# Optimization experiments

Hardware: AMD Instinct MI355X
Metric: run time of the kernel (lower is better)

Reference implementation:

```python
import jax, jax.numpy as jnp
import numpy as np

B, S, D_IN, D_OUT = 4, 2048, 4096, 4096


def setup_inputs() -> dict:
    key = jax.random.key(0)
    k1, k2, k3, k4 = jax.random.split(key, 4)
    x = jax.random.normal(k1, (B, S, D_IN), dtype=jnp.float32)
    # int8-valued weights stored as int32 (values in [-127, 127])
    weight_int8 = jax.random.randint(k2, (D_OUT, D_IN), -127, 128, dtype=jnp.int32)
    # per-output-channel scale, strictly positive (abs-max / 127 style)
    scale = jax.random.uniform(k3, (D_OUT, 1), dtype=jnp.float32, minval=1e-4, maxval=2e-2)
    bias = jax.random.normal(k4, (D_OUT,), dtype=jnp.float32)
    return {"x": x, "weight_int8": weight_int8, "scale": scale, "bias": bias}


def reference(x, weight_int8, scale, bias):
    # Dequantize: per-output-row scale applied to int8 weights -> fp32 [O, I]
    w = weight_int8.astype(jnp.float32) * scale
    # F.linear: y = x @ w^T + b
    out = jnp.einsum('bsi,oi->bso', x, w) + bias
    return out
```

## Files before the change

### kernel.cpp

```cpp
#include <hip/hip_runtime.h>
#include <cstdint>
#include <cstddef>

typedef int i32x4 __attribute__((ext_vector_type(4)));

#define BM 256
#define BN 256
#define BK 64

__device__ __forceinline__ void load16_to_lds(const void* g, void* l) {
  __builtin_amdgcn_global_load_lds(
      (const __attribute__((address_space(1))) void*)g,
      (__attribute__((address_space(3))) void*)l,
      16, 0, 0);
}

__global__ __launch_bounds__(256) void quant_xw(const float* __restrict__ x,
                                                char* __restrict__ xq,
                                                float* __restrict__ sx,
                                                const int* __restrict__ w,
                                                char* __restrict__ wq,
                                                int M, int K) {
  const int t = threadIdx.x;
  __shared__ float red[4];
  if ((int)blockIdx.x < M) {
    const int row = blockIdx.x;
    const float* xr = x + (size_t)row * K;
    float4 v[4];
    float amax = 0.f;
#pragma unroll
    for (int j = 0; j < 4; ++j) {
      v[j] = ((const float4*)xr)[t + j * 256];
      amax = fmaxf(amax, fmaxf(fmaxf(fabsf(v[j].x), fabsf(v[j].y)),
                               fmaxf(fabsf(v[j].z), fabsf(v[j].w))));
    }
#pragma unroll
    for (int off = 32; off; off >>= 1)
      amax = fmaxf(amax, __shfl_xor(amax, off));
    if ((t & 63) == 0) red[t >> 6] = amax;
    __syncthreads();
    amax = fmaxf(fmaxf(red[0], red[1]), fmaxf(red[2], red[3]));
    amax = fmaxf(amax, 1e-20f);

    const float s = 127.0f / amax;
    int* outw = (int*)(xq + (size_t)row * K);
#pragma unroll
    for (int j = 0; j < 4; ++j) {
      int q0 = __float2int_rn(v[j].x * s);
      int q1 = __float2int_rn(v[j].y * s);
      int q2 = __float2int_rn(v[j].z * s);
      int q3 = __float2int_rn(v[j].w * s);
      int pk = (q0 & 0xff) | ((q1 & 0xff) << 8) | ((q2 & 0xff) << 16) | ((q3 & 0xff) << 24);
      outw[t + j * 256] = pk;
    }
    if (t == 0) sx[row] = amax * (1.0f / 127.0f);
  } else {
    const size_t base = (size_t)(blockIdx.x - M) * 4096;
    int* outw = (int*)(wq + base);
#pragma unroll
    for (int j = 0; j < 4; ++j) {
      const int c = t + j * 256;
      int4 a = ((const int4*)(w + base))[c];
      outw[c] = (a.x & 0xff) | ((a.y & 0xff) << 8) | ((a.z & 0xff) << 16) | ((a.w & 0xff) << 24);
    }
  }
}

__global__ __launch_bounds__(512) void gemm_i8_bt(const char* __restrict__ A,
                                                  const char* __restrict__ Bw,
                                                  const float* __restrict__ sx,
                                                  const float* __restrict__ sw,
                                                  const float* __restrict__ bias,
                                                  float* __restrict__ out,
                                                  int M, int N, int K) {
  __shared__ __align__(16) char As[3][BM * BK];
  __shared__ __align__(16) char Bs[3][BN * BK];

  const int tid  = threadIdx.x;
  const int wave = tid >> 6;
  const int lane = tid & 63;
  const int wm   = wave >> 2;
  const int wn   = wave & 3;

  const int gx   = N / BN;
  const int nwg  = gx * (M / BM);
  const int orig = blockIdx.y * gx + blockIdx.x;
  const int wg   = (orig & 7) * (nwg >> 3) + (orig >> 3);
  const int bn   = wg % gx;
  const int bm   = wg / gx;

  i32x4 acc[8][4] = {};

  const int rowT = tid >> 2;
  const int jg   = ((tid & 3) ^ ((tid >> 3) & 3)) << 4;
  const char* Ag1 = A  + (size_t)(bm * BM + rowT) * K + jg;
  const char* Ag2 = Ag1 + (size_t)128 * K;
  const char* Bg1 = Bw + (size_t)(bn * BN + rowT) * K + jg;
  const char* Bg2 = Bg1 + (size_t)128 * K;

  const int ldsO1 = wave << 10;
  const int ldsO2 = 8192 + (wave << 10);

  const int fr  = lane & 15;
  const int swz = (((lane >> 4) ^ ((fr >> 1) & 3)) << 4);
  int offA[8], offB[4];
#pragma unroll
  for (int m = 0; m < 8; ++m) offA[m] = (wm * 128 + m * 16 + fr) * 64 + swz;
#pragma unroll
  for (int n = 0; n < 4; ++n) offB[n] = (wn * 64 + n * 16 + fr) * 64 + swz;

  const int NT = K / BK;

  load16_to_lds(Ag1,      &As[0][ldsO1]);
  load16_to_lds(Ag2,      &As[0][ldsO2]);
  load16_to_lds(Bg1,      &Bs[0][ldsO1]);
  load16_to_lds(Bg2,      &Bs[0][ldsO2]);
  load16_to_lds(Ag1 + BK, &As[1][ldsO1]);
  load16_to_lds(Ag2 + BK, &As[1][ldsO2]);
  load16_to_lds(Bg1 + BK, &Bs[1][ldsO1]);
  load16_to_lds(Bg2 + BK, &Bs[1][ldsO2]);
  asm volatile("s_waitcnt vmcnt(4)" ::: "memory");
  __builtin_amdgcn_s_barrier();

  int buf = 0;
  for (int t = 0; t < NT; ++t) {
    const int  nb = (buf >= 1) ? buf - 1 : 2;
    const size_t ko = (size_t)(t + 2) * BK;
    const bool pf = (t + 2) < NT;

    i32x4 af0 = *(const i32x4*)&As[buf][offA[0]];
    i32x4 af1 = *(const i32x4*)&As[buf][offA[1]];
    i32x4 af2 = *(const i32x4*)&As[buf][offA[2]];
    i32x4 af3 = *(const i32x4*)&As[buf][offA[3]];
    i32x4 bf0 = *(const i32x4*)&Bs[buf][offB[0]];
    i32x4 bf1 = *(const i32x4*)&Bs[buf][offB[1]];
    i32x4 bf2 = *(const i32x4*)&Bs[buf][offB[2]];
    i32x4 bf3 = *(const i32x4*)&Bs[buf][offB[3]];
    if (pf) {
      load16_to_lds(Ag1 + ko, &As[nb][ldsO1]);
      load16_to_lds(Ag2 + ko, &As[nb][ldsO2]);
    }
    __builtin_amdgcn_s_barrier();
    asm volatile("s_waitcnt lgkmcnt(0)" ::: "memory");
    __builtin_amdgcn_sched_barrier(0);
    __builtin_amdgcn_s_setprio(1);
    acc[0][0] = __builtin_amdgcn_mfma_i32_16x16x64_i8(af0, bf0, acc[0][0], 0, 0, 0);
    acc[0][1] = __builtin_amdgcn_mfma_i32_16x16x64_i8(af0, bf1, acc[0][1], 0, 0, 0);
    acc[0][2] = __builtin_amdgcn_mfma_i32_16x16x64_i8(af0, bf2, acc[0][2], 0, 0, 0);
    acc[0][3] = __builtin_amdgcn_mfma_i32_16x16x64_i8(af0, bf3, acc[0][3], 0, 0, 0);
    acc[1][0] = __builtin_amdgcn_mfma_i32_16x16x64_i8(af1, bf0, acc[1][0], 0, 0, 0);
    acc[1][1] = __builtin_amdgcn_mfma_i32_16x16x64_i8(af1, bf1, acc[1][1], 0, 0, 0);
    acc[1][2] = __builtin_amdgcn_mfma_i32_16x16x64_i8(af1, bf2, acc[1][2], 0, 0, 0);
    acc[1][3] = __builtin_amdgcn_mfma_i32_16x16x64_i8(af1, bf3, acc[1][3], 0, 0, 0);
    acc[2][0] = __builtin_amdgcn_mfma_i32_16x16x64_i8(af2, bf0, acc[2][0], 0, 0, 0);
    acc[2][1] = __builtin_amdgcn_mfma_i32_16x16x64_i8(af2, bf1, acc[2][1], 0, 0, 0);
    acc[2][2] = __builtin_amdgcn_mfma_i32_16x16x64_i8(af2, bf2, acc[2][2], 0, 0, 0);
    acc[2][3] = __builtin_amdgcn_mfma_i32_16x16x64_i8(af2, bf3, acc[2][3], 0, 0, 0);
    acc[3][0] = __builtin_amdgcn_mfma_i32_16x16x64_i8(af3, bf0, acc[3][0], 0, 0, 0);
    acc[3][1] = __builtin_amdgcn_mfma_i32_16x16x64_i8(af3, bf1, acc[3][1], 0, 0, 0);
    acc[3][2] = __builtin_amdgcn_mfma_i32_16x16x64_i8(af3, bf2, acc[3][2], 0, 0, 0);
    acc[3][3] = __builtin_amdgcn_mfma_i32_16x16x64_i8(af3, bf3, acc[3][3], 0, 0, 0);
    __builtin_amdgcn_s_setprio(0);
    __builtin_amdgcn_s_barrier();

    i32x4 af4 = *(const i32x4*)&As[buf][offA[4]];
    i32x4 af5 = *(const i32x4*)&As[buf][offA[5]];
    i32x4 af6 = *(const i32x4*)&As[buf][offA[6]];
    i32x4 af7 = *(const i32x4*)&As[buf][offA[7]];
    if (pf) {
      load16_to_lds(Bg1 + ko, &Bs[nb][ldsO1]);
      load16_to_lds(Bg2 + ko, &Bs[nb][ldsO2]);
    }
    __builtin_amdgcn_s_barrier();
    asm volatile("s_waitcnt lgkmcnt(0)" ::: "memory");
    __builtin_amdgcn_sched_barrier(0);
    __builtin_amdgcn_s_setprio(1);
    acc[4][0] = __builtin_amdgcn_mfma_i32_16x16x64_i8(af4, bf0, acc[4][0], 0, 0, 0);
    acc[4][1] = __builtin_amdgcn_mfma_i32_16x16x64_i8(af4, bf1, acc[4][1], 0, 0, 0);
    acc[4][2] = __builtin_amdgcn_mfma_i32_16x16x64_i8(af4, bf2, acc[4][2], 0, 0, 0);
    acc[4][3] = __builtin_amdgcn_mfma_i32_16x16x64_i8(af4, bf3, acc[4][3], 0, 0, 0);
    acc[5][0] = __builtin_amdgcn_mfma_i32_16x16x64_i8(af5, bf0, acc[5][0], 0, 0, 0);
    acc[5][1] = __builtin_amdgcn_mfma_i32_16x16x64_i8(af5, bf1, acc[5][1], 0, 0, 0);
    acc[5][2] = __builtin_amdgcn_mfma_i32_16x16x64_i8(af5, bf2, acc[5][2], 0, 0, 0);
    acc[5][3] = __builtin_amdgcn_mfma_i32_16x16x64_i8(af5, bf3, acc[5][3], 0, 0, 0);
    acc[6][0] = __builtin_amdgcn_mfma_i32_16x16x64_i8(af6, bf0, acc[6][0], 0, 0, 0);
    acc[6][1] = __builtin_amdgcn_mfma_i32_16x16x64_i8(af6, bf1, acc[6][1], 0, 0, 0);
    acc[6][2] = __builtin_amdgcn_mfma_i32_16x16x64_i8(af6, bf2, acc[6][2], 0, 0, 0);
    acc[6][3] = __builtin_amdgcn_mfma_i32_16x16x64_i8(af6, bf3, acc[6][3], 0, 0, 0);
    acc[7][0] = __builtin_amdgcn_mfma_i32_16x16x64_i8(af7, bf0, acc[7][0], 0, 0, 0);
    acc[7][1] = __builtin_amdgcn_mfma_i32_16x16x64_i8(af7, bf1, acc[7][1], 0, 0, 0);
    acc[7][2] = __builtin_amdgcn_mfma_i32_16x16x64_i8(af7, bf2, acc[7][2], 0, 0, 0);
    acc[7][3] = __builtin_amdgcn_mfma_i32_16x16x64_i8(af7, bf3, acc[7][3], 0, 0, 0);
    __builtin_amdgcn_s_setprio(0);

    if (pf)                 { asm volatile("s_waitcnt vmcnt(4)" ::: "memory"); }
    else if (t + 1 < NT)    { asm volatile("s_waitcnt vmcnt(0)" ::: "memory"); }
    __builtin_amdgcn_s_barrier();

    buf = (buf < 2) ? buf + 1 : 0;
  }

  const int colc = lane & 15;
  const int rq   = (lane >> 4) << 2;
  float sxv[8][4];
#pragma unroll
  for (int m = 0; m < 8; ++m) {
    const int row0 = bm * BM + wm * 128 + m * 16 + rq;
#pragma unroll
    for (int r = 0; r < 4; ++r) sxv[m][r] = sx[row0 + r];
  }
#pragma unroll
  for (int n = 0; n < 4; ++n) {
    const int col = bn * BN + wn * 64 + n * 16 + colc;
    const float sc = sw[col];
    const float bi = bias[col];
#pragma unroll
    for (int m = 0; m < 8; ++m) {
      const int row0 = bm * BM + wm * 128 + m * 16 + rq;
#pragma unroll
      for (int r = 0; r < 4; ++r)
        out[(size_t)(row0 + r) * N + col] = (float)acc[m][n][r] * (sxv[m][r] * sc) + bi;
    }
  }
}

extern "C" void kernel_launch(void* const* d_in, const int* in_sizes, int n_in,
                              void* d_out, int out_size, void* d_ws, size_t ws_size,
                              hipStream_t stream) {
  const float* x     = (const float*)d_in[0];
  const int*   w     = (const int*)d_in[1];
  const float* scale = (const float*)d_in[2];
  const float* bias  = (const float*)d_in[3];
  float*       out   = (float*)d_out;

  const int N = in_sizes[3];
  const int K = in_sizes[1] / N;
  const int M = in_sizes[0] / K;

  char*  xq = (char*)d_ws;
  char*  wq = xq + (size_t)M * K;
  float* sx = (float*)(wq + (size_t)N * K);

  const unsigned wblocks = (unsigned)(((size_t)N * K) / 4096);
  quant_xw<<<dim3((unsigned)M + wblocks), dim3(256), 0, stream>>>(x, xq, sx, w, wq, M, K);

  gemm_i8_bt<<<dim3(N / BN, M / BM), dim3(512), 0, stream>>>(xq, wq, sx, scale, bias, out, M, N, K);
}
```

Before: 414.8 us.

## Switch int8 GEMM inner loop to 32x32x32 MFMA instructions

Replaces the 16x16x64 int8 MFMA tiling with 32x32x32 MFMA. Each wave now holds a 4x2 grid of 32x32 accumulators, and the K=64 tile is split into two K=32 halves across the two compute phases. The goal is fewer MFMA issues and fewer LDS fragment reads per tile, since the larger instruction has higher operand reuse. The LDS read offsets, swizzle and epilogue row mapping are rewritten to match the 32x32 output layout. The epilogue now reloads the row scale per element.

```diff
diff --git a/kernel.cpp b/kernel.cpp
--- a/kernel.cpp
+++ b/kernel.cpp
@@ -2,7 +2,8 @@
 #include <cstdint>
 #include <cstddef>
 
-typedef int i32x4 __attribute__((ext_vector_type(4)));
+typedef int i32x4  __attribute__((ext_vector_type(4)));
+typedef int i32x16 __attribute__((ext_vector_type(16)));
 
 #define BM 256
 #define BN 256
@@ -89,7 +90,7 @@
   const int bn   = wg % gx;
   const int bm   = wg / gx;
 
-  i32x4 acc[8][4] = {};
+  i32x16 acc[4][2] = {};
 
   const int rowT = tid >> 2;
   const int jg   = ((tid & 3) ^ ((tid >> 3) & 3)) << 4;
@@ -101,13 +102,20 @@
   const int ldsO1 = wave << 10;
   const int ldsO2 = 8192 + (wave << 10);
 
-  const int fr  = lane & 15;
-  const int swz = (((lane >> 4) ^ ((fr >> 1) & 3)) << 4);
-  int offA[8], offB[4];
-#pragma unroll
-  for (int m = 0; m < 8; ++m) offA[m] = (wm * 128 + m * 16 + fr) * 64 + swz;
-#pragma unroll
-  for (int n = 0; n < 4; ++n) offB[n] = (wn * 64 + n * 16 + fr) * 64 + swz;
+  const int fr = lane & 31;
+  const int jj = lane >> 5;
+  const int st = (fr >> 1) & 3;
+  int offA[4][2], offB[2][2];
+#pragma unroll
+  for (int m = 0; m < 4; ++m)
+#pragma unroll
+    for (int s = 0; s < 2; ++s)
+      offA[m][s] = (wm * 128 + m * 32 + fr) * 64 + (((s * 2 + jj) ^ st) << 4);
+#pragma unroll
+  for (int n = 0; n < 2; ++n)
+#pragma unroll
+    for (int s = 0; s < 2; ++s)
+      offB[n][s] = (wn * 64 + n * 32 + fr) * 64 + (((s * 2 + jj) ^ st) << 4);
 
   const int NT = K / BK;
 
@@ -128,14 +136,12 @@
     const size_t ko = (size_t)(t + 2) * BK;
     const bool pf = (t + 2) < NT;
 
-    i32x4 af0 = *(const i32x4*)&As[buf][offA[0]];
-    i32x4 af1 = *(const i32x4*)&As[buf][offA[1]];
-    i32x4 af2 = *(const i32x4*)&As[buf][offA[2]];
-    i32x4 af3 = *(const i32x4*)&As[buf][offA[3]];
-    i32x4 bf0 = *(const i32x4*)&Bs[buf][offB[0]];
-    i32x4 bf1 = *(const i32x4*)&Bs[buf][offB[1]];
-    i32x4 bf2 = *(const i32x4*)&Bs[buf][offB[2]];
-    i32x4 bf3 = *(const i32x4*)&Bs[buf][offB[3]];
+    i32x4 a00 = *(const i32x4*)&As[buf][offA[0][0]];
+    i32x4 a01 = *(const i32x4*)&As[buf][offA[1][0]];
+    i32x4 a02 = *(const i32x4*)&As[buf][offA[2][0]];
+    i32x4 a03 = *(const i32x4*)&As[buf][offA[3][0]];
+    i32x4 b00 = *(const i32x4*)&Bs[buf][offB[0][0]];
+    i32x4 b01 = *(const i32x4*)&Bs[buf][offB[1][0]];
     if (pf) {
       load16_to_lds(Ag1 + ko, &As[nb][ldsO1]);
       load16_to_lds(Ag2 + ko, &As[nb][ldsO2]);
@@ -143,30 +149,24 @@
     __builtin_amdgcn_s_barrier();
     asm volatile("s_waitcnt lgkmcnt(0)" ::: "memory");
     __builtin_amdgcn_sched_barrier(0);
+    i32x4 a10 = *(const i32x4*)&As[buf][offA[0][1]];
+    i32x4 a11 = *(const i32x4*)&As[buf][offA[1][1]];
+    i32x4 a12 = *(const i32x4*)&As[buf][offA[2][1]];
+    i32x4 a13 = *(const i32x4*)&As[buf][offA[3][1]];
+    i32x4 b10 = *(const i32x4*)&Bs[buf][offB[0][1]];
+    i32x4 b11 = *(const i32x4*)&Bs[buf][offB[1][1]];
     __builtin_amdgcn_s_setprio(1);
-    acc[0][0] = __builtin_amdgcn_mfma_i32_16x16x64_i8(af0, bf0, acc[0][0], 0, 0, 0);
-    acc[0][1] = __builtin_amdgcn_mfma_i32_16x16x64_i8(af0, bf1, acc[0][1], 0, 0, 0);
-    acc[0][2] = __builtin_amdgcn_mfma_i32_16x16x64_i8(af0, bf2, acc[0][2], 0, 0, 0);
-    acc[0][3] = __builtin_amdgcn_mfma_i32_16x16x64_i8(af0, bf3, acc[0][3], 0, 0, 0);
-    acc[1][0] = __builtin_amdgcn_mfma_i32_16x16x64_i8(af1, bf0, acc[1][0], 0, 0, 0);
-    acc[1][1] = __builtin_amdgcn_mfma_i32_16x16x64_i8(af1, bf1, acc[1][1], 0, 0, 0);
-    acc[1][2] = __builtin_amdgcn_mfma_i32_16x16x64_i8(af1, bf2, acc[1][2], 0, 0, 0);
-    acc[1][3] = __builtin_amdgcn_mfma_i32_16x16x64_i8(af1, bf3, acc[1][3], 0, 0, 0);
-    acc[2][0] = __builtin_amdgcn_mfma_i32_16x16x64_i8(af2, bf0, acc[2][0], 0, 0, 0);
-    acc[2][1] = __builtin_amdgcn_mfma_i32_16x16x64_i8(af2, bf1, acc[2][1], 0, 0, 0);
-    acc[2][2] = __builtin_amdgcn_mfma_i32_16x16x64_i8(af2, bf2, acc[2][2], 0, 0, 0);
-    acc[2][3] = __builtin_amdgcn_mfma_i32_16x16x64_i8(af2, bf3, acc[2][3], 0, 0, 0);
-    acc[3][0] = __builtin_amdgcn_mfma_i32_16x16x64_i8(af3, bf0, acc[3][0], 0, 0, 0);
-    acc[3][1] = __builtin_amdgcn_mfma_i32_16x16x64_i8(af3, bf1, acc[3][1], 0, 0, 0);
-    acc[3][2] = __builtin_amdgcn_mfma_i32_16x16x64_i8(af3, bf2, acc[3][2], 0, 0, 0);
-    acc[3][3] = __builtin_amdgcn_mfma_i32_16x16x64_i8(af3, bf3, acc[3][3], 0, 0, 0);
+    acc[0][0] = __builtin_amdgcn_mfma_i32_32x32x32_i8(a00, b00, acc[0][0], 0, 0, 0);
+    acc[0][1] = __builtin_amdgcn_mfma_i32_32x32x32_i8(a00, b01, acc[0][1], 0, 0, 0);
+    acc[1][0] = __builtin_amdgcn_mfma_i32_32x32x32_i8(a01, b00, acc[1][0], 0, 0, 0);
+    acc[1][1] = __builtin_amdgcn_mfma_i32_32x32x32_i8(a01, b01, acc[1][1], 0, 0, 0);
+    acc[2][0] = __builtin_amdgcn_mfma_i32_32x32x32_i8(a02, b00, acc[2][0], 0, 0, 0);
+    acc[2][1] = __builtin_amdgcn_mfma_i32_32x32x32_i8(a02, b01, acc[2][1], 0, 0, 0);
+    acc[3][0] = __builtin_amdgcn_mfma_i32_32x32x32_i8(a03, b00, acc[3][0], 0, 0, 0);
+    acc[3][1] = __builtin_amdgcn_mfma_i32_32x32x32_i8(a03, b01, acc[3][1], 0, 0, 0);
     __builtin_amdgcn_s_setprio(0);
     __builtin_amdgcn_s_barrier();
 
-    i32x4 af4 = *(const i32x4*)&As[buf][offA[4]];
-    i32x4 af5 = *(const i32x4*)&As[buf][offA[5]];
-    i32x4 af6 = *(const i32x4*)&As[buf][offA[6]];
-    i32x4 af7 = *(const i32x4*)&As[buf][offA[7]];
     if (pf) {
       load16_to_lds(Bg1 + ko, &Bs[nb][ldsO1]);
       load16_to_lds(Bg2 + ko, &Bs[nb][ldsO2]);
@@ -175,22 +175,14 @@
     asm volatile("s_waitcnt lgkmcnt(0)" ::: "memory");
     __builtin_amdgcn_sched_barrier(0);
     __builtin_amdgcn_s_setprio(1);
-    acc[4][0] = __builtin_amdgcn_mfma_i32_16x16x64_i8(af4, bf0, acc[4][0], 0, 0, 0);
-    acc[4][1] = __builtin_amdgcn_mfma_i32_16x16x64_i8(af4, bf1, acc[4][1], 0, 0, 0);
-    acc[4][2] = __builtin_amdgcn_mfma_i32_16x16x64_i8(af4, bf2, acc[4][2], 0, 0, 0);
-    acc[4][3] = __builtin_amdgcn_mfma_i32_16x16x64_i8(af4, bf3, acc[4][3], 0, 0, 0);
-    acc[5][0] = __builtin_amdgcn_mfma_i32_16x16x64_i8(af5, bf0, acc[5][0], 0, 0, 0);
-    acc[5][1] = __builtin_amdgcn_mfma_i32_16x16x64_i8(af5, bf1, acc[5][1], 0, 0, 0);
-    acc[5][2] = __builtin_amdgcn_mfma_i32_16x16x64_i8(af5, bf2, acc[5][2], 0, 0, 0);
-    acc[5][3] = __builtin_amdgcn_mfma_i32_16x16x64_i8(af5, bf3, acc[5][3], 0, 0, 0);
-    acc[6][0] = __builtin_amdgcn_mfma_i32_16x16x64_i8(af6, bf0, acc[6][0], 0, 0, 0);
-    acc[6][1] = __builtin_amdgcn_mfma_i32_16x16x64_i8(af6, bf1, acc[6][1], 0, 0, 0);
-    acc[6][2] = __builtin_amdgcn_mfma_i32_16x16x64_i8(af6, bf2, acc[6][2], 0, 0, 0);
-    acc[6][3] = __builtin_amdgcn_mfma_i32_16x16x64_i8(af6, bf3, acc[6][3], 0, 0, 0);
-    acc[7][0] = __builtin_amdgcn_mfma_i32_16x16x64_i8(af7, bf0, acc[7][0], 0, 0, 0);
-    acc[7][1] = __builtin_amdgcn_mfma_i32_16x16x64_i8(af7, bf1, acc[7][1], 0, 0, 0);
-    acc[7][2] = __builtin_amdgcn_mfma_i32_16x16x64_i8(af7, bf2, acc[7][2], 0, 0, 0);
-    acc[7][3] = __builtin_amdgcn_mfma_i32_16x16x64_i8(af7, bf3, acc[7][3], 0, 0, 0);
+    acc[0][0] = __builtin_amdgcn_mfma_i32_32x32x32_i8(a10, b10, acc[0][0], 0, 0, 0);
+    acc[0][1] = __builtin_amdgcn_mfma_i32_32x32x32_i8(a10, b11, acc[0][1], 0, 0, 0);
+    acc[1][0] = __builtin_amdgcn_mfma_i32_32x32x32_i8(a11, b10, acc[1][0], 0, 0, 0);
+    acc[1][1] = __builtin_amdgcn_mfma_i32_32x32x32_i8(a11, b11, acc[1][1], 0, 0, 0);
+    acc[2][0] = __builtin_amdgcn_mfma_i32_32x32x32_i8(a12, b10, acc[2][0], 0, 0, 0);
+    acc[2][1] = __builtin_amdgcn_mfma_i32_32x32x32_i8(a12, b11, acc[2][1], 0, 0, 0);
+    acc[3][0] = __builtin_amdgcn_mfma_i32_32x32x32_i8(a13, b10, acc[3][0], 0, 0, 0);
+    acc[3][1] = __builtin_amdgcn_mfma_i32_32x32x32_i8(a13, b11, acc[3][1], 0, 0, 0);
     __builtin_amdgcn_s_setprio(0);
 
     if (pf)                 { asm volatile("s_waitcnt vmcnt(4)" ::: "memory"); }
@@ -200,26 +192,21 @@
     buf = (buf < 2) ? buf + 1 : 0;
   }
 
-  const int colc = lane & 15;
-  const int rq   = (lane >> 4) << 2;
-  float sxv[8][4];
-#pragma unroll
-  for (int m = 0; m < 8; ++m) {
-    const int row0 = bm * BM + wm * 128 + m * 16 + rq;
-#pragma unroll
-    for (int r = 0; r < 4; ++r) sxv[m][r] = sx[row0 + r];
-  }
-#pragma unroll
-  for (int n = 0; n < 4; ++n) {
-    const int col = bn * BN + wn * 64 + n * 16 + colc;
-    const float sc = sw[col];
-    const float bi = bias[col];
-#pragma unroll
-    for (int m = 0; m < 8; ++m) {
-      const int row0 = bm * BM + wm * 128 + m * 16 + rq;
-#pragma unroll
-      for (int r = 0; r < 4; ++r)
-        out[(size_t)(row0 + r) * N + col] = (float)acc[m][n][r] * (sxv[m][r] * sc) + bi;
+  const int colc = lane & 31;
+  const int rhi  = (lane >> 5) << 2;
+  const int col0 = bn * BN + wn * 64 + colc;
+  const float sc0 = sw[col0],      bi0 = bias[col0];
+  const float sc1 = sw[col0 + 32], bi1 = bias[col0 + 32];
+#pragma unroll
+  for (int m = 0; m < 4; ++m) {
+    const int row0 = bm * BM + wm * 128 + m * 32 + rhi;
+#pragma unroll
+    for (int r = 0; r < 16; ++r) {
+      const int row = row0 + (r & 3) + ((r >> 2) << 3);
+      const float srow = sx[row];
+      float* op = out + (size_t)row * N + col0;
+      op[0]  = (float)acc[m][0][r] * (srow * sc0) + bi0;
+      op[32] = (float)acc[m][1][r] * (srow * sc1) + bi1;
     }
   }
 }
```

New measurement: 431.2 us. 1.04x slower.
